# Performance work log

Hardware: AMD Instinct MI355X
Metric: run time of the kernel (lower is better)

The kernel has to match this reference:

```python
import jax, jax.numpy as jnp
import numpy as np

D_EMBED = 1024
N_HEADS = 16
D_HEAD = 64
D_MLP = 4096
SEQ = 2048
BATCH = 2
ALPHA = 1.0


def setup_inputs() -> dict:
    key = jax.random.key(0)
    ks = jax.random.split(key, 7)
    s = ALPHA / np.sqrt(D_EMBED)
    return {
        "x": jax.random.normal(ks[0], (BATCH, SEQ, D_EMBED), jnp.float32),
        "W_K": s * jax.random.normal(ks[1], (N_HEADS, D_HEAD, D_EMBED), jnp.float32),
        "W_Q": s * jax.random.normal(ks[2], (N_HEADS, D_HEAD, D_EMBED), jnp.float32),
        "W_V": s * jax.random.normal(ks[3], (N_HEADS, D_HEAD, D_EMBED), jnp.float32),
        "W_O": s * jax.random.normal(ks[4], (D_EMBED, N_HEADS * D_HEAD), jnp.float32),
        "W_in": s * jax.random.normal(ks[5], (D_MLP, D_EMBED), jnp.float32),
        "b_in": jnp.zeros((D_MLP,), jnp.float32),
        "W_out": s * jax.random.normal(ks[6], (D_EMBED, D_MLP), jnp.float32),
        "b_out": jnp.zeros((D_EMBED,), jnp.float32),
    }


def reference(x, W_K, W_Q, W_V, W_O, W_in, b_in, W_out, b_out):
    b, c_len, _ = x.shape
    d_head = W_K.shape[1]
    # q/k/v: [batch, head, ctx, d_head]
    k = jnp.einsum('ahe,bce->bach', W_K, x)
    q = jnp.einsum('ahe,bce->bach', W_Q, x)
    v = jnp.einsum('ahe,bce->bach', W_V, x)
    # scores[b,a,c,C] = k_c . q_C  (faithful to original index convention)
    scores = jnp.einsum('bach,baCh->bacC', k, q)
    mask = jnp.tril(jnp.ones((c_len, c_len), dtype=x.dtype))  # [c, C]
    masked = scores * mask - 1e10 * (1.0 - mask)
    attn = jax.nn.softmax(masked / np.sqrt(d_head), axis=-1)  # softmax over C (query idx)
    # z[b,a,C,h] = sum_c v[b,a,c,h] * attn[b,a,c,C]
    z = jnp.einsum('bach,bacC->baCh', v, attn)
    z_flat = jnp.transpose(z, (0, 2, 1, 3)).reshape(b, c_len, -1)  # [b, c, a*h]
    attn_out = jnp.einsum('ef,bcf->bce', W_O, z_flat)
    x = x + attn_out
    h = jnp.einsum('me,bce->bcm', W_in, x) + b_in
    h = jax.nn.relu(h)
    mlp_out = jnp.einsum('em,bcm->bce', W_out, h) + b_out
    return x + mlp_out
```

## Files before the change

### kernel.cpp

```cpp
#include <hip/hip_runtime.h>
#include <hip/hip_bf16.h>
#include <cstdint>
#include <cstddef>

typedef __bf16 bf16;
typedef bf16 bf16x4 __attribute__((ext_vector_type(4)));
typedef bf16 bf16x8 __attribute__((ext_vector_type(8)));
typedef float floatx4 __attribute__((ext_vector_type(4)));
typedef float floatx16 __attribute__((ext_vector_type(16)));
typedef unsigned int uint;

#define MFMA16(a, b, c) __builtin_amdgcn_mfma_f32_16x16x32_bf16((a), (b), (c), 0, 0, 0)
#define MFMA32(a, b, c) __builtin_amdgcn_mfma_f32_32x32x16_bf16((a), (b), (c), 0, 0, 0)

#define K2 0.18033688011112042f

__device__ __forceinline__ void async16(const void* g, void* l) {
    __builtin_amdgcn_global_load_lds((const __attribute__((address_space(1))) void*)g,
                                     (__attribute__((address_space(3))) void*)l,
                                     16, 0, 0);
}

__device__ __forceinline__ void stage64s(const bf16* g0, int ldg, bf16* lds, int wave, int lane) {
#pragma unroll
    for (int i = 0; i < 2; ++i) {
        int r0 = wave * 16 + i * 8;
        async16(g0 + (size_t)(r0 + (lane >> 3)) * ldg + ((lane & 7) ^ (lane >> 3)) * 8,
                lds + r0 * 64);
    }
}
__device__ __forceinline__ void stage64q(const bf16* g0, int ldg, bf16* lds, int wave, int lane) {
    int r0 = wave * 8;
    async16(g0 + (size_t)(r0 + (lane >> 3)) * ldg + ((lane & 7) ^ (lane >> 3)) * 8,
            lds + r0 * 64);
}
__device__ __forceinline__ bf16x8 rd64(const bf16* t, int row, int chunk) {
    return *(const bf16x8*)&t[row * 64 + ((chunk ^ (row & 7)) * 8)];
}
__device__ __forceinline__ bf16x8 rd32(const bf16* t, int row, int quad) {
    return *(const bf16x8*)&t[row * 32 + ((quad ^ (row & 3)) * 8)];
}

__device__ __forceinline__ uint pk2(float lo, float hi) {
    union { bf16 h[2]; uint u; } c;
    c.h[0] = (bf16)lo;
    c.h[1] = (bf16)hi;
    return c.u;
}

__global__ __launch_bounds__(256) void cvt_all(const float* __restrict__ x,
                                               const float* __restrict__ WQ,
                                               const float* __restrict__ WK,
                                               const float* __restrict__ WV,
                                               const float* __restrict__ WO,
                                               const float* __restrict__ Win,
                                               const float* __restrict__ Wout,
                                               bf16* __restrict__ xb,
                                               bf16* __restrict__ wqkv,
                                               bf16* __restrict__ wo,
                                               bf16* __restrict__ win,
                                               bf16* __restrict__ wout) {
    int blk = blockIdx.x;
    const float* src;
    bf16* dst;
    int off;
    if (blk < 1024)      { src = WQ;   dst = wqkv;           off = blk; }
    else if (blk < 2048) { src = WK;   dst = wqkv + 1048576; off = blk - 1024; }
    else if (blk < 3072) { src = WV;   dst = wqkv + 2097152; off = blk - 2048; }
    else if (blk < 4096) { src = WO;   dst = wo;             off = blk - 3072; }
    else if (blk < 8192) { src = Win;  dst = win;            off = blk - 4096; }
    else if (blk < 12288){ src = Wout; dst = wout;           off = blk - 8192; }
    else                 { src = x;    dst = xb;             off = blk - 12288; }
    int i = off * 1024 + threadIdx.x * 4;
    float4 v = *(const float4*)(src + i);
    bf16x4 o = {(bf16)v.x, (bf16)v.y, (bf16)v.z, (bf16)v.w};
    *(bf16x4*)(dst + i) = o;
}

template <int EPI, int NACC>
__device__ __forceinline__ void epilogue(floatx4 (&acc)[4][NACC], int m0, int n0,
                                         int wm, int wn, int col, int quad,
                                         float* Cf, bf16* Cb, int ldc,
                                         const float* bias, const float* res) {
#pragma unroll
    for (int mi = 0; mi < 4; ++mi)
#pragma unroll
        for (int ni = 0; ni < NACC; ++ni)
#pragma unroll
            for (int r = 0; r < 4; ++r) {
                int row = m0 + wm + mi * 16 + quad * 4 + r;
                int cc = n0 + wn + ni * 16 + col;
                size_t idx = (size_t)row * ldc + cc;
                float v = acc[mi][ni][r];
                if constexpr (EPI == 0) {
                    Cb[idx] = (bf16)v;
                } else if constexpr (EPI == 1) {
                    v += res[idx];
                    Cf[idx] = v;
                    Cb[idx] = (bf16)v;
                } else if constexpr (EPI == 2) {
                    v += bias[cc];
                    v = fmaxf(v, 0.f);
                    Cb[idx] = (bf16)v;
                } else {
                    v += bias[cc] + Cf[idx];
                    Cf[idx] = v;
                }
            }
}

template <int EPI>
__global__ __launch_bounds__(256) void gemm_pipe(const bf16* __restrict__ A, int lda,
                                                 const bf16* __restrict__ B, int ldb, int K,
                                                 float* __restrict__ Cf, bf16* __restrict__ Cb,
                                                 int ldc, const float* __restrict__ bias,
                                                 const float* __restrict__ res) {
    __shared__ __align__(16) bf16 As[3][128 * 32];
    __shared__ __align__(16) bf16 Bs[3][128 * 32];
    const int tid = threadIdx.x, wave = tid >> 6, lane = tid & 63;
    const int m0 = blockIdx.y * 128, n0 = blockIdx.x * 128;
    const int wm = (wave >> 1) * 64, wn = (wave & 1) * 64;
    const int col = lane & 15, quad = lane >> 4;
    const int cs8 = ((lane & 3) ^ ((lane >> 2) & 3)) * 8;

    floatx4 acc[4][4];
#pragma unroll
    for (int mi = 0; mi < 4; ++mi)
#pragma unroll
        for (int ni = 0; ni < 4; ++ni) acc[mi][ni] = (floatx4){0.f, 0.f, 0.f, 0.f};

    auto stage = [&](int buf, int k0) {
#pragma unroll
        for (int i = 0; i < 2; ++i) {
            int r0 = wave * 32 + i * 16;
            async16(A + (size_t)(m0 + r0 + (lane >> 2)) * lda + k0 + cs8,
                    As[buf] + r0 * 32);
            async16(B + (size_t)(n0 + r0 + (lane >> 2)) * ldb + k0 + cs8,
                    Bs[buf] + r0 * 32);
        }
    };

    const int nk = K / 32;
    stage(0, 0);
    stage(1, 32);
    for (int it = 0; it < nk; ++it) {
        if (it + 1 < nk) asm volatile("s_waitcnt vmcnt(4)" ::: "memory");
        else             asm volatile("s_waitcnt vmcnt(0)" ::: "memory");
        __builtin_amdgcn_s_barrier();
        if (it + 2 < nk) stage((it + 2) % 3, (it + 2) * 32);

        const bf16* as = As[it % 3];
        const bf16* bs = Bs[it % 3];
        bf16x8 af[4], bfr[4];
#pragma unroll
        for (int mi = 0; mi < 4; ++mi) af[mi] = rd32(as, wm + mi * 16 + col, quad);
#pragma unroll
        for (int ni = 0; ni < 4; ++ni) bfr[ni] = rd32(bs, wn + ni * 16 + col, quad);
#pragma unroll
        for (int mi = 0; mi < 4; ++mi)
#pragma unroll
            for (int ni = 0; ni < 4; ++ni)
                acc[mi][ni] = MFMA16(af[mi], bfr[ni], acc[mi][ni]);
    }
    epilogue<EPI, 4>(acc, m0, n0, wm, wn, col, quad, Cf, Cb, ldc, bias, res);
}

__global__ __launch_bounds__(256) void gemm_sk(const bf16* __restrict__ A, int lda,
                                               const bf16* __restrict__ B, int ldb, int Kh,
                                               float* __restrict__ P) {
    __shared__ __align__(16) bf16 As[3][128 * 32];
    __shared__ __align__(16) bf16 Bs[3][128 * 32];
    const int tid = threadIdx.x, wave = tid >> 6, lane = tid & 63;
    const int m0 = blockIdx.y * 128, n0 = blockIdx.x * 128;
    A += (size_t)blockIdx.z * Kh;
    B += (size_t)blockIdx.z * Kh;
    P += (size_t)blockIdx.z * 4096 * 1024;
    const int wm = (wave >> 1) * 64, wn = (wave & 1) * 64;
    const int col = lane & 15, quad = lane >> 4;
    const int cs8 = ((lane & 3) ^ ((lane >> 2) & 3)) * 8;

    floatx4 acc[4][4];
#pragma unroll
    for (int mi = 0; mi < 4; ++mi)
#pragma unroll
        for (int ni = 0; ni < 4; ++ni) acc[mi][ni] = (floatx4){0.f, 0.f, 0.f, 0.f};

    auto stage = [&](int buf, int k0) {
#pragma unroll
        for (int i = 0; i < 2; ++i) {
            int r0 = wave * 32 + i * 16;
            async16(A + (size_t)(m0 + r0 + (lane >> 2)) * lda + k0 + cs8,
                    As[buf] + r0 * 32);
            async16(B + (size_t)(n0 + r0 + (lane >> 2)) * ldb + k0 + cs8,
                    Bs[buf] + r0 * 32);
        }
    };

    const int nk = Kh / 32;
    stage(0, 0);
    stage(1, 32);
    for (int it = 0; it < nk; ++it) {
        if (it + 1 < nk) asm volatile("s_waitcnt vmcnt(4)" ::: "memory");
        else             asm volatile("s_waitcnt vmcnt(0)" ::: "memory");
        __builtin_amdgcn_s_barrier();
        if (it + 2 < nk) stage((it + 2) % 3, (it + 2) * 32);

        const bf16* as = As[it % 3];
        const bf16* bs = Bs[it % 3];
        bf16x8 af[4], bfr[4];
#pragma unroll
        for (int mi = 0; mi < 4; ++mi) af[mi] = rd32(as, wm + mi * 16 + col, quad);
#pragma unroll
        for (int ni = 0; ni < 4; ++ni) bfr[ni] = rd32(bs, wn + ni * 16 + col, quad);
        __builtin_amdgcn_s_setprio(1);
#pragma unroll
        for (int mi = 0; mi < 4; ++mi)
#pragma unroll
            for (int ni = 0; ni < 4; ++ni)
                acc[mi][ni] = MFMA16(af[mi], bfr[ni], acc[mi][ni]);
        __builtin_amdgcn_s_setprio(0);
    }
#pragma unroll
    for (int mi = 0; mi < 4; ++mi)
#pragma unroll
        for (int ni = 0; ni < 4; ++ni)
#pragma unroll
            for (int r = 0; r < 4; ++r) {
                int row = m0 + wm + mi * 16 + quad * 4 + r;
                int cc = n0 + wn + ni * 16 + col;
                P[(size_t)row * 1024 + cc] = acc[mi][ni][r];
            }
}

__global__ __launch_bounds__(256) void mlp2_reduce(const float* __restrict__ p0,
                                                   const float* __restrict__ p1,
                                                   const float* __restrict__ bout,
                                                   float* __restrict__ out) {
    int i = (blockIdx.x * 256 + threadIdx.x) * 4;
    float4 a = *(const float4*)(p0 + i);
    float4 b = *(const float4*)(p1 + i);
    float4 o = *(const float4*)(out + i);
    float4 bb = *(const float4*)(bout + (i & 1023));
    o.x += a.x + b.x + bb.x;
    o.y += a.y + b.y + bb.y;
    o.z += a.z + b.z + bb.z;
    o.w += a.w + b.w + bb.w;
    *(float4*)(out + i) = o;
}

template <int EPI>
__global__ __launch_bounds__(256) void gemm_pipe64(const bf16* __restrict__ A, int lda,
                                                   const bf16* __restrict__ B, int ldb, int K,
                                                   float* __restrict__ Cf, bf16* __restrict__ Cb,
                                                   int ldc, const float* __restrict__ bias,
                                                   const float* __restrict__ res) {
    __shared__ __align__(16) bf16 As[3][128 * 64];
    __shared__ __align__(16) bf16 Bs[3][64 * 64];
    const int tid = threadIdx.x, wave = tid >> 6, lane = tid & 63;
    const int orig = blockIdx.y * 16 + blockIdx.x;
    const int wgid = (orig & 7) * 64 + (orig >> 3);
    const int m0 = (wgid >> 4) * 128, n0 = (wgid & 15) * 64;
    const int wm = (wave >> 1) * 64, wn = (wave & 1) * 32;
    const int col = lane & 15, quad = lane >> 4;
    const int rsub = lane >> 3;
    const int csub = ((lane & 7) ^ rsub) * 8;

    floatx4 acc[4][2];
#pragma unroll
    for (int mi = 0; mi < 4; ++mi)
#pragma unroll
        for (int ni = 0; ni < 2; ++ni) acc[mi][ni] = (floatx4){0.f, 0.f, 0.f, 0.f};

    auto stage = [&](int buf, int k0) {
#pragma unroll
        for (int i = 0; i < 4; ++i) {
            int r0 = wave * 32 + i * 8;
            async16(A + (size_t)(m0 + r0 + rsub) * lda + k0 + csub, As[buf] + r0 * 64);
        }
#pragma unroll
        for (int i = 0; i < 2; ++i) {
            int r0 = wave * 16 + i * 8;
            async16(B + (size_t)(n0 + r0 + rsub) * ldb + k0 + csub, Bs[buf] + r0 * 64);
        }
    };

    const int nk = K / 64;
    stage(0, 0);
    stage(1, 64);
    for (int it = 0; it < nk; ++it) {
        if (it + 1 < nk) asm volatile("s_waitcnt vmcnt(6)" ::: "memory");
        else             asm volatile("s_waitcnt vmcnt(0)" ::: "memory");
        __builtin_amdgcn_s_barrier();
        if (it + 2 < nk) stage((it + 2) % 3, (it + 2) * 64);

        const bf16* as = As[it % 3];
        const bf16* bs = Bs[it % 3];
#pragma unroll
        for (int ks = 0; ks < 2; ++ks) {
            bf16x8 af[4], bfr[2];
#pragma unroll
            for (int mi = 0; mi < 4; ++mi) {
                int row = wm + mi * 16 + col;
                af[mi] = *(const bf16x8*)&as[row * 64 + (((ks * 4 + quad) ^ (row & 7)) * 8)];
            }
#pragma unroll
            for (int ni = 0; ni < 2; ++ni) {
                int row = wn + ni * 16 + col;
                bfr[ni] = *(const bf16x8*)&bs[row * 64 + (((ks * 4 + quad) ^ (row & 7)) * 8)];
            }
#pragma unroll
            for (int mi = 0; mi < 4; ++mi)
#pragma unroll
                for (int ni = 0; ni < 2; ++ni)
                    acc[mi][ni] = MFMA16(af[mi], bfr[ni], acc[mi][ni]);
        }
    }
    epilogue<EPI, 2>(acc, m0, n0, wm, wn, col, quad, Cf, Cb, ldc, bias, res);
}

__global__ __launch_bounds__(256) void transpose_v(const bf16* __restrict__ qkv,
                                                   const float* __restrict__ linv,
                                                   bf16* __restrict__ vt) {
    __shared__ bf16 t[64][65];
    const int bh = blockIdx.y, ct = blockIdx.x;
    const int b = bh >> 4, a = bh & 15;
    const float* lv = linv + (size_t)bh * 2048 + ct * 64;
    for (int idx = threadIdx.x; idx < 4096; idx += 256) {
        int c = idx >> 6, h = idx & 63;
        float v = (float)qkv[(size_t)(b * 2048 + ct * 64 + c) * 3072 + 2048 + a * 64 + h];
        t[h][c] = (bf16)(v * lv[c]);
    }
    __syncthreads();
    for (int idx = threadIdx.x; idx < 4096; idx += 256) {
        int h = idx >> 6, c = idx & 63;
        vt[(size_t)(bh * 64 + h) * 2048 + ct * 64 + c] = t[h][c];
    }
}

__global__ __launch_bounds__(512, 4) void attn_stats(const bf16* __restrict__ qkv,
                                                     float* __restrict__ linv) {
    __shared__ __align__(16) bf16 Kt[128 * 64];
    __shared__ __align__(16) bf16 Qt[3][64 * 64];
    __shared__ float red[4][32];
    const int xx = blockIdx.x;
    const int t = (xx & 1) ? (15 - (xx >> 1)) : (xx >> 1);
    const int bh = blockIdx.y;
    const int b = bh >> 4, a = bh & 15;
    const int tid = threadIdx.x, wave = tid >> 6, lane = tid & 63;
    const int l31 = lane & 31, lh = lane >> 5;
    const int kq = wave & 3, qh = wave >> 2;
    const bf16* base = qkv + (size_t)b * 2048 * 3072;
    const int c0 = t * 128;
    const int niter = 2 * t + 2;

    stage64s(base + (size_t)c0 * 3072 + 1024 + a * 64, 3072, Kt, wave, lane);
    stage64q(base + a * 64, 3072, Qt[0], wave, lane);
    stage64q(base + (size_t)64 * 3072 + a * 64, 3072, Qt[1], wave, lane);

    float lrun[16];
#pragma unroll
    for (int r = 0; r < 16; ++r) lrun[r] = 0.f;
    bf16x8 kf[4];

    for (int i = 0; i < niter; ++i) {
        if (i + 1 < niter) asm volatile("s_waitcnt vmcnt(1)" ::: "memory");
        else               asm volatile("s_waitcnt vmcnt(0)" ::: "memory");
        __builtin_amdgcn_s_barrier();
        if (i + 2 < niter)
            stage64q(base + (size_t)(i + 2) * 64 * 3072 + a * 64, 3072,
                     Qt[(i + 2) % 3], wave, lane);
        if (i == 0) {
#pragma unroll
            for (int s = 0; s < 4; ++s) kf[s] = rd64(Kt, 32 * kq + l31, 2 * s + lh);
        }
        const bf16* q = Qt[i % 3];
        bf16x8 qf0 = rd64(q, 32 * qh + l31, 0 + lh);
        bf16x8 qf1 = rd64(q, 32 * qh + l31, 2 + lh);
        bf16x8 qf2 = rd64(q, 32 * qh + l31, 4 + lh);
        bf16x8 qf3 = rd64(q, 32 * qh + l31, 6 + lh);
        floatx16 s0 = (floatx16)0.f, s1 = (floatx16)0.f;
        __builtin_amdgcn_s_setprio(1);
        s0 = MFMA32(kf[0], qf0, s0);
        s1 = MFMA32(kf[2], qf2, s1);
        s0 = MFMA32(kf[1], qf1, s0);
        s1 = MFMA32(kf[3], qf3, s1);
        __builtin_amdgcn_s_setprio(0);
#pragma unroll
        for (int r = 0; r < 16; ++r) {
            float e = __builtin_amdgcn_exp2f((s0[r] + s1[r]) * K2);
            if (i >= niter - 2) {
                int Crel = 64 * (i - 2 * t) + 32 * qh + l31;
                int crel = 32 * kq + (r & 3) + 8 * (r >> 2) + 4 * lh;
                if (Crel > crel) e = 0.f;
            }
            lrun[r] += e;
        }
    }
#pragma unroll
    for (int r = 0; r < 16; ++r) {
        float v = lrun[r];
        v += __shfl_xor(v, 1);
        v += __shfl_xor(v, 2);
        v += __shfl_xor(v, 4);
        v += __shfl_xor(v, 8);
        v += __shfl_xor(v, 16);
        lrun[r] = v;
    }
    if (qh == 1 && l31 == 0) {
#pragma unroll
        for (int r = 0; r < 16; ++r)
            red[kq][(r & 3) + 8 * (r >> 2) + 4 * lh] = lrun[r];
    }
    __syncthreads();
    if (qh == 0 && l31 == 0) {
#pragma unroll
        for (int r = 0; r < 16; ++r) {
            int cr = (r & 3) + 8 * (r >> 2) + 4 * lh;
            linv[(size_t)bh * 2048 + c0 + 32 * kq + cr] = 1.0f / (lrun[r] + red[kq][cr]);
        }
    }
}

__global__ __launch_bounds__(512, 4) void attn_av(const bf16* __restrict__ qkv,
                                                  const bf16* __restrict__ vt,
                                                  bf16* __restrict__ zb) {
    __shared__ __align__(16) char smem[65536];
    bf16* Qt = (bf16*)smem;
    bf16* Kt = (bf16*)(smem + 16384);
    bf16* Vt = (bf16*)(smem + 40960);
    const int xx = blockIdx.x;
    const int t = (xx & 1) ? (15 - (xx >> 1)) : (xx >> 1);
    const int bh = blockIdx.y;
    const int b = bh >> 4, a = bh & 15;
    const int tid = threadIdx.x, wave = tid >> 6, lane = tid & 63;
    const int l31 = lane & 31, lh = lane >> 5;
    const int Cq = wave & 3, cq = wave >> 2;
    const bf16* base = qkv + (size_t)b * 2048 * 3072;
    const int C0 = t * 128;
    const int niter = 32 - 2 * t;

    stage64s(base + (size_t)C0 * 3072 + a * 64, 3072, Qt, wave, lane);
    stage64q(base + (size_t)(2 * t) * 64 * 3072 + 1024 + a * 64, 3072, Kt, wave, lane);
    stage64q(vt + (size_t)bh * 64 * 2048 + 2 * t * 64, 2048, Vt, wave, lane);
    stage64q(base + (size_t)(2 * t + 1) * 64 * 3072 + 1024 + a * 64, 3072, Kt + 4096, wave, lane);
    stage64q(vt + (size_t)bh * 64 * 2048 + (2 * t + 1) * 64, 2048, Vt + 4096, wave, lane);

    floatx16 zacc[2];
    zacc[0] = (floatx16)0.f;
    zacc[1] = (floatx16)0.f;
    bf16x8 qf[4];

    for (int i = 0; i < niter; ++i) {
        const int ct = 2 * t + i;
        if (i + 1 < niter) asm volatile("s_waitcnt vmcnt(2)" ::: "memory");
        else               asm volatile("s_waitcnt vmcnt(0)" ::: "memory");
        __builtin_amdgcn_s_barrier();
        if (i + 2 < niter) {
            stage64q(base + (size_t)(ct + 2) * 64 * 3072 + 1024 + a * 64, 3072,
                     Kt + ((i + 2) % 3) * 4096, wave, lane);
            stage64q(vt + (size_t)bh * 64 * 2048 + (ct + 2) * 64, 2048,
                     Vt + ((i + 2) % 3) * 4096, wave, lane);
        }
        if (i == 0) {
#pragma unroll
            for (int s = 0; s < 4; ++s) qf[s] = rd64(Qt, 32 * Cq + l31, 2 * s + lh);
        }
        const bf16* kt = Kt + (i % 3) * 4096;
        const bf16* vts = Vt + (i % 3) * 4096;

        floatx16 s0 = (floatx16)0.f, s1 = (floatx16)0.f;
        __builtin_amdgcn_s_setprio(1);
        s0 = MFMA32(rd64(kt, 32 * cq + l31, 0 + lh), qf[0], s0);
        s1 = MFMA32(rd64(kt, 32 * cq + l31, 4 + lh), qf[2], s1);
        s0 = MFMA32(rd64(kt, 32 * cq + l31, 2 + lh), qf[1], s0);
        s1 = MFMA32(rd64(kt, 32 * cq + l31, 6 + lh), qf[3], s1);
        __builtin_amdgcn_s_setprio(0);

        float p[16];
#pragma unroll
        for (int r = 0; r < 16; ++r) {
            float e = __builtin_amdgcn_exp2f((s0[r] + s1[r]) * K2);
            if (i < 2) {
                int Crel = 32 * Cq + l31;
                int crel = 64 * i + 32 * cq + (r & 3) + 8 * (r >> 2) + 4 * lh;
                if (Crel > crel) e = 0.f;
            }
            p[r] = e;
        }

        bf16x8 pa[2];
#pragma unroll
        for (int g = 0; g < 2; ++g) {
            uint w0 = pk2(p[8 * g + 0], p[8 * g + 1]);
            uint w1 = pk2(p[8 * g + 2], p[8 * g + 3]);
            uint w2 = pk2(p[8 * g + 4], p[8 * g + 5]);
            uint w3 = pk2(p[8 * g + 6], p[8 * g + 7]);
            uint xw0 = (uint)__shfl_xor((int)w0, 32);
            uint xw1 = (uint)__shfl_xor((int)w1, 32);
            uint xw2 = (uint)__shfl_xor((int)w2, 32);
            uint xw3 = (uint)__shfl_xor((int)w3, 32);
            union { uint u[4]; bf16x8 v; } cv;
            cv.u[0] = lh ? xw2 : w0;
            cv.u[1] = lh ? xw3 : w1;
            cv.u[2] = lh ? w2 : xw0;
            cv.u[3] = lh ? w3 : xw1;
            pa[g] = cv.v;
        }

        __builtin_amdgcn_s_setprio(1);
#pragma unroll
        for (int ht = 0; ht < 2; ++ht) {
#pragma unroll
            for (int s = 0; s < 2; ++s) {
                bf16x8 vf = rd64(vts, 32 * ht + l31, 4 * cq + 2 * s + lh);
                zacc[ht] = MFMA32(pa[s], vf, zacc[ht]);
            }
        }
        __builtin_amdgcn_s_setprio(0);
    }

    __syncthreads();
    float* Zex = (float*)smem;
    if (cq == 1) {
#pragma unroll
        for (int ht = 0; ht < 2; ++ht)
#pragma unroll
            for (int q = 0; q < 4; ++q) {
                float4 t4 = {zacc[ht][4 * q + 0], zacc[ht][4 * q + 1],
                             zacc[ht][4 * q + 2], zacc[ht][4 * q + 3]};
                *(float4*)&Zex[Cq * 2048 + lane * 32 + (((ht * 4 + q) ^ (lane & 7)) * 4)] = t4;
            }
    }
    __syncthreads();
    if (cq == 0) {
#pragma unroll
        for (int ht = 0; ht < 2; ++ht)
#pragma unroll
            for (int q = 0; q < 4; ++q) {
                float4 t4 = *(const float4*)&Zex[Cq * 2048 + lane * 32 +
                                                 (((ht * 4 + q) ^ (lane & 7)) * 4)];
                zacc[ht][4 * q + 0] += t4.x;
                zacc[ht][4 * q + 1] += t4.y;
                zacc[ht][4 * q + 2] += t4.z;
                zacc[ht][4 * q + 3] += t4.w;
            }
#pragma unroll
        for (int ht = 0; ht < 2; ++ht)
#pragma unroll
            for (int r = 0; r < 16; ++r) {
                int Cg = C0 + 32 * Cq + (r & 3) + 8 * (r >> 2) + 4 * lh;
                zb[(size_t)(b * 2048 + Cg) * 1024 + a * 64 + 32 * ht + l31] =
                    (bf16)zacc[ht][r];
            }
    }
}

extern "C" void kernel_launch(void* const* d_in, const int* in_sizes, int n_in,
                              void* d_out, int out_size, void* d_ws, size_t ws_size,
                              hipStream_t stream) {
    (void)in_sizes; (void)n_in; (void)out_size; (void)ws_size;
    const float* x    = (const float*)d_in[0];
    const float* WK   = (const float*)d_in[1];
    const float* WQ   = (const float*)d_in[2];
    const float* WV   = (const float*)d_in[3];
    const float* WO   = (const float*)d_in[4];
    const float* Win  = (const float*)d_in[5];
    const float* bin  = (const float*)d_in[6];
    const float* Wout = (const float*)d_in[7];
    const float* bout = (const float*)d_in[8];
    float* out = (float*)d_out;

    char* ws = (char*)d_ws;
    bf16*  xb   = (bf16*)(ws + 0);
    bf16*  wqkv = (bf16*)(ws + 8388608);
    bf16*  wo   = (bf16*)(ws + 14680064);
    bf16*  win  = (bf16*)(ws + 16777216);
    bf16*  wout = (bf16*)(ws + 25165824);
    bf16*  qkvb = (bf16*)(ws + 33554432);
    bf16*  vtb  = (bf16*)(ws + 58720256);
    float* mst  = (float*)(ws + 67108864);
    bf16*  zbuf = (bf16*)(ws + 67633152);
    bf16*  xmid = (bf16*)(ws + 76021760);
    bf16*  hbuf = (bf16*)(ws + 84410368);
    float* part = (float*)(ws + 33554432);

    cvt_all<<<16384, 256, 0, stream>>>(x, WQ, WK, WV, WO, Win, Wout,
                                       xb, wqkv, wo, win, wout);

    gemm_pipe<0><<<dim3(24, 32), 256, 0, stream>>>(xb, 1024, wqkv, 1024, 1024,
                                                   nullptr, qkvb, 3072, nullptr, nullptr);
    attn_stats<<<dim3(16, 32), 512, 0, stream>>>(qkvb, mst);
    transpose_v<<<dim3(32, 32), 256, 0, stream>>>(qkvb, mst, vtb);
    attn_av<<<dim3(16, 32), 512, 0, stream>>>(qkvb, vtb, zbuf);
    gemm_pipe64<1><<<dim3(16, 32), 256, 0, stream>>>(zbuf, 1024, wo, 1024, 1024,
                                                     out, xmid, 1024, nullptr, x);
    gemm_pipe<2><<<dim3(32, 32), 256, 0, stream>>>(xmid, 1024, win, 1024, 1024,
                                                   nullptr, hbuf, 4096, bin, nullptr);
    gemm_sk<<<dim3(8, 32, 2), 256, 0, stream>>>(hbuf, 4096, wout, 4096, 2048, part);
    mlp2_reduce<<<4096, 256, 0, stream>>>(part, part + 4194304, bout, out);
}
```

Baseline: 380.4 us.

## Use 256x256 eight-wave tiles for MLP-in and drop split-K for MLP-out

A new gemm_8p kernel computes 256x256 output tiles with 8 waves, and uses grid swizzling. It stages A and B in separate phases with an extra barrier between the two halves of the M sub-tile. It replaces the 128x128 gemm_pipe used for the W_in projection, aiming for more operand reuse per LDS load. The W_out projection now runs as a single full-K gemm_pipe64 with an accumulating epilogue (EPI 3), removing the split-K partial buffers and the separate reduce kernel. The trade-off is fewer blocks and less parallelism on the final GEMM, plus higher register and LDS pressure in the large-tile kernel.

Result: no change. 375.0 us (-1.4%).

```diff
diff --git a/kernel.cpp b/kernel.cpp
--- a/kernel.cpp
+++ b/kernel.cpp
@@ -165,87 +165,113 @@
     epilogue<EPI, 4>(acc, m0, n0, wm, wn, col, quad, Cf, Cb, ldc, bias, res);
 }
 
-__global__ __launch_bounds__(256) void gemm_sk(const bf16* __restrict__ A, int lda,
-                                               const bf16* __restrict__ B, int ldb, int Kh,
-                                               float* __restrict__ P) {
-    __shared__ __align__(16) bf16 As[3][128 * 32];
-    __shared__ __align__(16) bf16 Bs[3][128 * 32];
+template <int EPI>
+__global__ __launch_bounds__(512, 2) void gemm_8p(const bf16* __restrict__ A, int lda,
+                                                  const bf16* __restrict__ B, int ldb, int K,
+                                                  float* __restrict__ Cf, bf16* __restrict__ Cb,
+                                                  int ldc, const float* __restrict__ bias,
+                                                  const float* __restrict__ res) {
+    __shared__ __align__(16) bf16 As[3][256 * 32];
+    __shared__ __align__(16) bf16 Bs[3][256 * 32];
     const int tid = threadIdx.x, wave = tid >> 6, lane = tid & 63;
-    const int m0 = blockIdx.y * 128, n0 = blockIdx.x * 128;
-    A += (size_t)blockIdx.z * Kh;
-    B += (size_t)blockIdx.z * Kh;
-    P += (size_t)blockIdx.z * 4096 * 1024;
-    const int wm = (wave >> 1) * 64, wn = (wave & 1) * 64;
+    const int gx = gridDim.x;
+    const int orig = blockIdx.y * gx + blockIdx.x;
+    const int cpx = (gx * gridDim.y) >> 3;
+    const int swz = (orig & 7) * cpx + (orig >> 3);
+    const int m0 = (swz % gx) * 256, n0 = (swz / gx) * 256;
+    const int wm = (wave >> 2) * 128, wn = (wave & 3) * 64;
     const int col = lane & 15, quad = lane >> 4;
     const int cs8 = ((lane & 3) ^ ((lane >> 2) & 3)) * 8;
 
-    floatx4 acc[4][4];
-#pragma unroll
-    for (int mi = 0; mi < 4; ++mi)
+    floatx4 acc[8][4];
+#pragma unroll
+    for (int mi = 0; mi < 8; ++mi)
 #pragma unroll
         for (int ni = 0; ni < 4; ++ni) acc[mi][ni] = (floatx4){0.f, 0.f, 0.f, 0.f};
 
-    auto stage = [&](int buf, int k0) {
+    auto stageA = [&](int buf, int k0) {
 #pragma unroll
         for (int i = 0; i < 2; ++i) {
             int r0 = wave * 32 + i * 16;
             async16(A + (size_t)(m0 + r0 + (lane >> 2)) * lda + k0 + cs8,
                     As[buf] + r0 * 32);
+        }
+    };
+    auto stageB = [&](int buf, int k0) {
+#pragma unroll
+        for (int i = 0; i < 2; ++i) {
+            int r0 = wave * 32 + i * 16;
             async16(B + (size_t)(n0 + r0 + (lane >> 2)) * ldb + k0 + cs8,
                     Bs[buf] + r0 * 32);
         }
     };
 
-    const int nk = Kh / 32;
-    stage(0, 0);
-    stage(1, 32);
+    const int nk = K / 32;
+    stageA(0, 0); stageB(0, 0);
+    stageA(1, 32); stageB(1, 32);
     for (int it = 0; it < nk; ++it) {
         if (it + 1 < nk) asm volatile("s_waitcnt vmcnt(4)" ::: "memory");
         else             asm volatile("s_waitcnt vmcnt(0)" ::: "memory");
         __builtin_amdgcn_s_barrier();
-        if (it + 2 < nk) stage((it + 2) % 3, (it + 2) * 32);
 
         const bf16* as = As[it % 3];
         const bf16* bs = Bs[it % 3];
-        bf16x8 af[4], bfr[4];
-#pragma unroll
-        for (int mi = 0; mi < 4; ++mi) af[mi] = rd32(as, wm + mi * 16 + col, quad);
+        const int pb = (it + 2) % 3;
+        const int pk = (it + 2) * 32;
+
+        if (it + 2 < nk) stageA(pb, pk);
+        bf16x8 bfr[4];
 #pragma unroll
         for (int ni = 0; ni < 4; ++ni) bfr[ni] = rd32(bs, wn + ni * 16 + col, quad);
-        __builtin_amdgcn_s_setprio(1);
-#pragma unroll
-        for (int mi = 0; mi < 4; ++mi)
-#pragma unroll
-            for (int ni = 0; ni < 4; ++ni)
-                acc[mi][ni] = MFMA16(af[mi], bfr[ni], acc[mi][ni]);
-        __builtin_amdgcn_s_setprio(0);
-    }
-#pragma unroll
-    for (int mi = 0; mi < 4; ++mi)
+        {
+            bf16x8 af[4];
+#pragma unroll
+            for (int mi = 0; mi < 4; ++mi) af[mi] = rd32(as, wm + mi * 16 + col, quad);
+            __builtin_amdgcn_s_setprio(1);
+#pragma unroll
+            for (int mi = 0; mi < 4; ++mi)
+#pragma unroll
+                for (int ni = 0; ni < 4; ++ni)
+                    acc[mi][ni] = MFMA16(af[mi], bfr[ni], acc[mi][ni]);
+            __builtin_amdgcn_s_setprio(0);
+        }
+        __builtin_amdgcn_s_barrier();
+
+        if (it + 2 < nk) stageB(pb, pk);
+        {
+            bf16x8 af[4];
+#pragma unroll
+            for (int mi = 0; mi < 4; ++mi)
+                af[mi] = rd32(as, wm + 64 + mi * 16 + col, quad);
+            __builtin_amdgcn_s_setprio(1);
+#pragma unroll
+            for (int mi = 0; mi < 4; ++mi)
+#pragma unroll
+                for (int ni = 0; ni < 4; ++ni)
+                    acc[mi + 4][ni] = MFMA16(af[mi], bfr[ni], acc[mi + 4][ni]);
+            __builtin_amdgcn_s_setprio(0);
+        }
+    }
+
+#pragma unroll
+    for (int mi = 0; mi < 8; ++mi)
 #pragma unroll
         for (int ni = 0; ni < 4; ++ni)
 #pragma unroll
             for (int r = 0; r < 4; ++r) {
                 int row = m0 + wm + mi * 16 + quad * 4 + r;
                 int cc = n0 + wn + ni * 16 + col;
-                P[(size_t)row * 1024 + cc] = acc[mi][ni][r];
-            }
-}
-
-__global__ __launch_bounds__(256) void mlp2_reduce(const float* __restrict__ p0,
-                                                   const float* __restrict__ p1,
-                                                   const float* __restrict__ bout,
-                                                   float* __restrict__ out) {
-    int i = (blockIdx.x * 256 + threadIdx.x) * 4;
-    float4 a = *(const float4*)(p0 + i);
-    float4 b = *(const float4*)(p1 + i);
-    float4 o = *(const float4*)(out + i);
-    float4 bb = *(const float4*)(bout + (i & 1023));
-    o.x += a.x + b.x + bb.x;
-    o.y += a.y + b.y + bb.y;
-    o.z += a.z + b.z + bb.z;
-    o.w += a.w + b.w + bb.w;
-    *(float4*)(out + i) = o;
+                size_t idx = (size_t)row * ldc + cc;
+                float v = acc[mi][ni][r];
+                if constexpr (EPI == 2) {
+                    v += bias[cc];
+                    v = fmaxf(v, 0.f);
+                    Cb[idx] = (bf16)v;
+                } else {
+                    Cb[idx] = (bf16)v;
+                }
+            }
+    (void)Cf; (void)res;
 }
 
 template <int EPI>
@@ -582,7 +608,6 @@
     bf16*  zbuf = (bf16*)(ws + 67633152);
     bf16*  xmid = (bf16*)(ws + 76021760);
     bf16*  hbuf = (bf16*)(ws + 84410368);
-    float* part = (float*)(ws + 33554432);
 
     cvt_all<<<16384, 256, 0, stream>>>(x, WQ, WK, WV, WO, Win, Wout,
                                        xb, wqkv, wo, win, wout);
@@ -594,8 +619,8 @@
     attn_av<<<dim3(16, 32), 512, 0, stream>>>(qkvb, vtb, zbuf);
     gemm_pipe64<1><<<dim3(16, 32), 256, 0, stream>>>(zbuf, 1024, wo, 1024, 1024,
                                                      out, xmid, 1024, nullptr, x);
-    gemm_pipe<2><<<dim3(32, 32), 256, 0, stream>>>(xmid, 1024, win, 1024, 1024,
-                                                   nullptr, hbuf, 4096, bin, nullptr);
-    gemm_sk<<<dim3(8, 32, 2), 256, 0, stream>>>(hbuf, 4096, wout, 4096, 2048, part);
-    mlp2_reduce<<<4096, 256, 0, stream>>>(part, part + 4194304, bout, out);
-}
+    gemm_8p<2><<<dim3(16, 16), 512, 0, stream>>>(xmid, 1024, win, 1024, 1024,
+                                                 nullptr, hbuf, 4096, bin, nullptr);
+    gemm_pipe64<3><<<dim3(16, 32), 256, 0, stream>>>(hbuf, 4096, wout, 4096, 4096,
+                                                     out, nullptr, 1024, bout, nullptr);
+}
```
